# Optimization experiments

Hardware: AMD Instinct MI355X
Metric: run time of the kernel (lower is better)

Reference implementation:

```python
import jax, jax.numpy as jnp
from jax import lax
import numpy as np

V = 30000   # vocab_size
E = 64      # embedding_dim
H = 64      # lstm_units
K = 9       # num_tags
B = 512
T = 512


def setup_inputs() -> dict:
    key = jax.random.key(0)
    ks = jax.random.split(key, 12)
    s = 0.05
    return {
        "tokens": jax.random.randint(ks[0], (B, T), 0, V),
        "emb":   jax.random.normal(ks[1], (V + 1, E), dtype=jnp.float32) * s,
        "Wf": jax.random.normal(ks[2], (E, 4 * H), dtype=jnp.float32) * s,
        "Uf": jax.random.normal(ks[3], (H, 4 * H), dtype=jnp.float32) * s,
        "bf": jnp.zeros((4 * H,), dtype=jnp.float32),
        "Wb": jax.random.normal(ks[4], (E, 4 * H), dtype=jnp.float32) * s,
        "Ub": jax.random.normal(ks[5], (H, 4 * H), dtype=jnp.float32) * s,
        "bb": jnp.zeros((4 * H,), dtype=jnp.float32),
        "Wd": jax.random.normal(ks[6], (2 * H, K), dtype=jnp.float32) * s,
        "bd": jnp.zeros((K,), dtype=jnp.float32),
        "trans": jax.random.normal(ks[7], (K, K), dtype=jnp.float32) * s,
    }


def _lstm(x_tm, mask_tm, W, U, b):
    """Keras-convention LSTM over time-major x_tm [T,B,E]; masked steps carry state."""
    Bsz = x_tm.shape[1]
    h0 = jnp.zeros((Bsz, U.shape[0]), x_tm.dtype)
    c0 = jnp.zeros_like(h0)

    def step(carry, inp):
        h, c = carry
        xt, mt = inp                      # xt [B,E], mt [B] bool
        z = xt @ W + h @ U + b            # [B,4H], gate order i,f,g,o
        i, f, g, o = jnp.split(z, 4, axis=-1)
        c_new = jax.nn.sigmoid(f) * c + jax.nn.sigmoid(i) * jnp.tanh(g)
        h_new = jax.nn.sigmoid(o) * jnp.tanh(c_new)
        m = mt[:, None]
        h2 = jnp.where(m, h_new, h)
        c2 = jnp.where(m, c_new, c)
        return (h2, c2), h2

    _, hs = lax.scan(step, (h0, c0), (x_tm, mask_tm))
    return hs                              # [T,B,H]


def _viterbi(pot, mask, trans):
    """Batched Viterbi decode. pot [B,T,K], mask [B,T] bool, trans [K,K]."""
    pot_t = pot.transpose(1, 0, 2)         # [T,B,K]
    m_t = mask.T                           # [T,B]
    alpha0 = pot_t[0]
    ident = jnp.arange(K, dtype=jnp.int32)[None, :]

    def step(alpha, inp):
        p, m = inp                         # p [B,K], m [B]
        scores = alpha[:, :, None] + trans[None]   # [B, prev K, next K]
        best = scores.max(axis=1)
        bp = scores.argmax(axis=1).astype(jnp.int32)
        mm = m[:, None]
        alpha_new = jnp.where(mm, best + p, alpha)
        bp = jnp.where(mm, bp, ident)
        return alpha_new, bp

    alpha, bps = lax.scan(step, alpha0, (pot_t[1:], m_t[1:]))   # bps [T-1,B,K]
    last = alpha.argmax(axis=-1).astype(jnp.int32)              # [B]

    def back(tag, bp):
        prev = jnp.take_along_axis(bp, tag[:, None], axis=1)[:, 0]
        return prev, prev

    _, ys = lax.scan(back, last, bps, reverse=True)             # ys[t] = tag_t, t<T-1
    tags = jnp.concatenate([ys, last[None]], axis=0).T          # [B,T]
    return jnp.where(mask, tags, 0)


def reference(tokens, emb, Wf, Uf, bf, Wb, Ub, bb, Wd, bd, trans):
    mask = tokens != 0                     # mask_zero semantics
    x = emb[tokens]                        # [B,T,E]
    x_tm = x.transpose(1, 0, 2)            # [T,B,E]
    m_tm = mask.T
    hf = _lstm(x_tm, m_tm, Wf, Uf, bf)                     # forward dir
    hb = _lstm(x_tm[::-1], m_tm[::-1], Wb, Ub, bb)[::-1]   # backward dir
    h = jnp.concatenate([hf, hb], axis=-1).transpose(1, 0, 2)  # [B,T,2H]
    potentials = h @ Wd + bd               # CRF emission potentials [B,T,K]
    decoded = _viterbi(potentials, mask, trans)
    seq_len = mask.sum(axis=1).astype(jnp.int32)
    return decoded, potentials, seq_len
```

## Files before the change

kernel.cpp:

```cpp
#include <hip/hip_runtime.h>

#define BB 512
#define TT 512
#define KK 9
#define VP1 30001
#define BTK ((size_t)BB * TT * KK)

typedef __attribute__((ext_vector_type(8))) short short8;
typedef __attribute__((ext_vector_type(4))) float float4v;

__device__ __forceinline__ float sigm(float x) {
    return __builtin_amdgcn_rcpf(1.0f + __expf(-x));
}
__device__ __forceinline__ float tanh_(float x) {
    return 1.0f - 2.0f * __builtin_amdgcn_rcpf(__expf(2.0f * x) + 1.0f);
}

__device__ __forceinline__ unsigned short f2bf(float f) {
    unsigned int u = __float_as_uint(f);
    unsigned int r = u + 0x7fffu + ((u >> 16) & 1u);
    return (unsigned short)(r >> 16);
}
__device__ __forceinline__ float bflo2f(unsigned int d) { return __uint_as_float(d << 16); }
__device__ __forceinline__ float bfhi2f(unsigned int d) { return __uint_as_float(d & 0xffff0000u); }

__device__ __forceinline__ float bcast(float v, int i) {
    return __uint_as_float(__builtin_amdgcn_readlane(__float_as_uint(v), i));
}

__device__ __forceinline__ void block_sync_lds() {
    __builtin_amdgcn_s_waitcnt(0xC07F);
    __builtin_amdgcn_s_barrier();
}

__global__ __launch_bounds__(256, 1)
void embw_kernel(const float* __restrict__ emb,
                 const float* __restrict__ Wf, const float* __restrict__ bfv,
                 const float* __restrict__ Wb, const float* __restrict__ bbv,
                 unsigned short* __restrict__ embw)
{
    const int v0 = blockIdx.x * 64;
    const int tid = threadIdx.x;
    const int w = tid >> 6, lane = tid & 63;
    const int l16 = lane & 15, quad = lane >> 4;

    __shared__ __align__(16) unsigned short sm[512 * 72];
    __shared__ float blds[512];
    unsigned short (*wlds)[72]  = (unsigned short(*)[72])sm;
    unsigned short (*clds)[520] = (unsigned short(*)[520])sm;

#pragma unroll
    for (int it = 0; it < 128; ++it) {
        int idx = it * 256 + tid;
        int dir = idx >> 14, rem = idx & 16383;
        int k = rem >> 8, scol = rem & 255;
        int u = scol & 63, g = scol >> 6;
        float val = (dir ? Wb : Wf)[k * 256 + scol];
        wlds[dir * 256 + u * 4 + g][k] = f2bf(val);
    }
    {
        int c = tid, c2 = tid + 256;
        int dir0 = c >> 8, rem0 = c & 255;
        blds[c] = (dir0 ? bbv : bfv)[(rem0 & 3) * 64 + (rem0 >> 2)];
        int dir1 = c2 >> 8, rem1 = c2 & 255;
        blds[c2] = (dir1 ? bbv : bfv)[(rem1 & 3) * 64 + (rem1 >> 2)];
    }

    short8 aFr[4][2];
#pragma unroll
    for (int mt = 0; mt < 4; ++mt) {
        int vrow = v0 + mt * 16 + l16;
        if (vrow >= VP1) vrow = VP1 - 1;
        const float* er = emb + (size_t)vrow * 64;
#pragma unroll
        for (int q = 0; q < 2; ++q) {
            const float* p = er + q * 32 + quad * 8;
            float4 x0 = *(const float4*)(p);
            float4 x1 = *(const float4*)(p + 4);
            short8 v;
            v[0] = (short)f2bf(x0.x); v[1] = (short)f2bf(x0.y);
            v[2] = (short)f2bf(x0.z); v[3] = (short)f2bf(x0.w);
            v[4] = (short)f2bf(x1.x); v[5] = (short)f2bf(x1.y);
            v[6] = (short)f2bf(x1.z); v[7] = (short)f2bf(x1.w);
            aFr[mt][q] = v;
        }
    }
    __syncthreads();

    short8 bFr[8][2];
    float biasn[8];
#pragma unroll
    for (int n = 0; n < 8; ++n) {
        int c = w * 128 + n * 16 + l16;
        biasn[n] = blds[c];
#pragma unroll
        for (int q = 0; q < 2; ++q)
            bFr[n][q] = *(const short8*)&wlds[c][q * 32 + quad * 8];
    }

    float4v acc[4][8];
#pragma unroll
    for (int mt = 0; mt < 4; ++mt)
#pragma unroll
        for (int n = 0; n < 8; ++n) {
            acc[mt][n][0] = biasn[n]; acc[mt][n][1] = biasn[n];
            acc[mt][n][2] = biasn[n]; acc[mt][n][3] = biasn[n];
        }
#pragma unroll
    for (int mt = 0; mt < 4; ++mt)
#pragma unroll
        for (int n = 0; n < 8; ++n) {
            acc[mt][n] = __builtin_amdgcn_mfma_f32_16x16x32_bf16(aFr[mt][0], bFr[n][0], acc[mt][n], 0, 0, 0);
            acc[mt][n] = __builtin_amdgcn_mfma_f32_16x16x32_bf16(aFr[mt][1], bFr[n][1], acc[mt][n], 0, 0, 0);
        }

    __syncthreads();

#pragma unroll
    for (int mt = 0; mt < 4; ++mt)
#pragma unroll
        for (int n = 0; n < 8; ++n) {
            int cc = w * 128 + n * 16 + l16;
#pragma unroll
            for (int r = 0; r < 4; ++r)
                clds[mt * 16 + quad * 4 + r][cc] = f2bf(acc[mt][n][r]);
        }
    __syncthreads();

#pragma unroll
    for (int it = 0; it < 16; ++it) {
        int idx = it * 256 + tid;
        int row = idx >> 6, chunk = idx & 63;
        if (v0 + row < VP1) {
            uint4 val = *(const uint4*)&clds[row][chunk * 8];
            *(uint4*)(embw + (size_t)(v0 + row) * 512 + chunk * 8) = val;
        }
    }
}

__global__ __launch_bounds__(256, 1)
void rec_kernel(const int* __restrict__ tokens,
                const unsigned short* __restrict__ embw,
                const float* __restrict__ Uf, const float* __restrict__ Ub,
                const float* __restrict__ Wd,
                float* __restrict__ potf, float* __restrict__ potb)
{
    const int blk = blockIdx.x;
    const int dir = blk >> 7;
    const int row0 = (blk & 127) * 4;
    const int tid = threadIdx.x;
    const int lane = tid & 63;
    const int w = tid >> 6;
    const int l16 = lane & 15, quad = lane >> 4;
    const int u = w * 16 + l16;

    const float* Up = dir ? Ub : Uf;
    float* pot = dir ? potb : potf;
    const uint2* ebase = (const uint2*)embw + dir * 64 + u;

    __shared__ int tokl[4][TT];
    __shared__ __align__(16) unsigned short hl[2][16][72];

    for (int i = tid; i < 2 * 16 * 72; i += 256)
        ((unsigned short*)hl)[i] = 0;
    for (int i = tid; i < 4 * TT; i += 256) {
        int r = i >> 9, t = i & 511;
        tokl[r][t] = tokens[(row0 + r) * TT + t];
    }

    short8 bU[4][2];
#pragma unroll
    for (int g = 0; g < 4; ++g)
#pragma unroll
        for (int q = 0; q < 2; ++q) {
            short8 v;
#pragma unroll
            for (int j = 0; j < 8; ++j) {
                int k = q * 32 + quad * 8 + j;
                v[j] = (short)f2bf(Up[k * 256 + g * 64 + u]);
            }
            bU[g][q] = v;
        }
    short8 bW[2];
#pragma unroll
    for (int q = 0; q < 2; ++q) {
        short8 v;
#pragma unroll
        for (int j = 0; j < 8; ++j) {
            int k = q * 32 + quad * 8 + j;
            v[j] = (l16 < KK) ? (short)f2bf(Wd[(dir * 64 + k) * KK + l16]) : (short)0;
        }
        bW[q] = v;
    }

    __syncthreads();

    int tokA[4], tokB[4];
    uint2 zxp[4];
#pragma unroll
    for (int d = 0; d < 4; ++d) {
        int td = dir ? (TT - 1 - d) : d;
        int td4 = dir ? (TT - 1 - (d + 4)) : (d + 4);
        tokA[d] = tokl[quad][td];
        tokB[d] = tokl[quad][td4];
    }
#pragma unroll
    for (int d = 0; d < 4; ++d)
        zxp[d] = ebase[(size_t)tokA[d] << 7];

    float c_st = 0.f, h_st = 0.f;

    float4v accg[4];
#pragma unroll
    for (int g = 0; g < 4; ++g) {
        accg[g][0] = 0.f; accg[g][1] = 0.f; accg[g][2] = 0.f; accg[g][3] = 0.f;
    }

    const int tprev0 = dir ? (w == 0 ? TT - 4 : TT - w) : (w == 0 ? 3 : w - 1);
    int vOff = (((row0 + quad) * TT + tprev0) * KK + l16) * 4;
    const int vStep = (dir ? -4 : 4) * KK * 4;

    for (int sb = 0; sb < TT; sb += 4) {
#pragma unroll
        for (int ss = 0; ss < 4; ++ss) {
            const int s = sb + ss;
            int tcur = tokA[ss];
            uint2 zcur = zxp[ss];

            hl[ss & 1][quad * 4][u] = f2bf(h_st);

            if (s + 4 < TT)
                zxp[ss] = ebase[(size_t)tokB[ss] << 7];
            tokA[ss] = tokB[ss];

            block_sync_lds();

            const unsigned short* hrow = &hl[ss & 1][l16][0];
            short8 a0 = *(const short8*)(hrow + quad * 8);
            short8 a1 = *(const short8*)(hrow + 32 + quad * 8);

            if (s + 8 < TT) {
                int t8 = dir ? (TT - 1 - (s + 8)) : (s + 8);
                tokB[ss] = tokl[quad][t8];
            }

            accg[0][0] = bflo2f(zcur.x);
            accg[1][0] = bfhi2f(zcur.x);
            accg[2][0] = bflo2f(zcur.y);
            accg[3][0] = bfhi2f(zcur.y);
#pragma unroll
            for (int g = 0; g < 4; ++g) {
                accg[g] = __builtin_amdgcn_mfma_f32_16x16x32_bf16(a0, bU[g][0], accg[g], 0, 0, 0);
                accg[g] = __builtin_amdgcn_mfma_f32_16x16x32_bf16(a1, bU[g][1], accg[g], 0, 0, 0);
            }

            if (w == ss && s > 0) {
                float4v accP = {0.f, 0.f, 0.f, 0.f};
                accP = __builtin_amdgcn_mfma_f32_16x16x32_bf16(a0, bW[0], accP, 0, 0, 0);
                accP = __builtin_amdgcn_mfma_f32_16x16x32_bf16(a1, bW[1], accP, 0, 0, 0);
                if (l16 < KK)
                    *(float*)((char*)pot + vOff) = accP[0];
                vOff += vStep;
            }

            {
                float zi = accg[0][0], zf = accg[1][0], zg = accg[2][0], zo = accg[3][0];
                float cn = sigm(zf) * c_st + sigm(zi) * tanh_(zg);
                float hn = sigm(zo) * tanh_(cn);
                bool m = (tcur != 0);
                h_st = m ? hn : h_st;
                c_st = m ? cn : c_st;
            }
        }
    }

    hl[0][quad * 4][u] = f2bf(h_st);
    block_sync_lds();
    if (w == 0) {
        const unsigned short* hrow = &hl[0][l16][0];
        short8 a0 = *(const short8*)(hrow + quad * 8);
        short8 a1 = *(const short8*)(hrow + 32 + quad * 8);
        float4v accP = {0.f, 0.f, 0.f, 0.f};
        accP = __builtin_amdgcn_mfma_f32_16x16x32_bf16(a0, bW[0], accP, 0, 0, 0);
        accP = __builtin_amdgcn_mfma_f32_16x16x32_bf16(a1, bW[1], accP, 0, 0, 0);
        int tlast = dir ? 0 : (TT - 1);
        if (l16 < KK)
            pot[((size_t)(row0 + quad) * TT + tlast) * KK + l16] = accP[0];
    }
}

__global__ __launch_bounds__(64)
void viterbi_kernel(const int* __restrict__ tokens,
                    const float* __restrict__ potf, const float* __restrict__ potb,
                    const float* __restrict__ bd, const float* __restrict__ trans,
                    float* __restrict__ dec_out, float* __restrict__ pot_out,
                    float* __restrict__ seq_out)
{
    const int row = blockIdx.x;
    const int lane = threadIdx.x;

    __shared__ float pl[TT * KK];
    __shared__ unsigned char bpl[(TT - 1) * KK];
    __shared__ unsigned char maskl[TT];
    __shared__ unsigned char segmap[64][KK];
    __shared__ unsigned char bseq[65];
    __shared__ float decl_[TT];
    __shared__ float bdl[16];

    if (lane < KK) bdl[lane] = bd[lane];

    int cnt = 0;
#pragma unroll
    for (int ch = 0; ch < TT / 64; ++ch) {
        int tk = tokens[row * TT + ch * 64 + lane];
        int m = (tk != 0) ? 1 : 0;
        maskl[ch * 64 + lane] = (unsigned char)m;
        cnt += m;
    }
    for (int off = 32; off > 0; off >>= 1) cnt += __shfl_down(cnt, off);
    if (lane == 0) seq_out[row] = (float)cnt;

    const size_t base = (size_t)row * (TT * KK);
    int r9 = lane % KK;
    for (int i = 0; i < (TT * KK) / 64; ++i) {
        int li = i * 64 + lane;
        float s = potf[base + li] + potb[base + li] + bdl[r9];
        pl[li] = s;
        pot_out[base + li] = s;
        r9 = (r9 + 1 == KK) ? 0 : r9 + 1;
    }
    __syncthreads();

    float treg[KK];
#pragma unroll
    for (int i = 0; i < KK; ++i) treg[i] = (lane < KK) ? trans[i * KK + lane] : 0.f;

    float alpha = (lane < KK) ? pl[lane] : -1e30f;
    float pnext = (lane < KK) ? pl[KK + lane] : 0.f;
    int mnext = maskl[1];
    for (int t = 1; t < TT; ++t) {
        float p = pnext;
        int m = mnext;
        if (t + 1 < TT) {
            pnext = (lane < KK) ? pl[(t + 1) * KK + lane] : 0.f;
            mnext = maskl[t + 1];
        }
        float sc[KK];
#pragma unroll
        for (int i = 0; i < KK; ++i) sc[i] = bcast(alpha, i) + treg[i];
        float b0 = sc[0]; int i0 = 0;
        if (sc[1] > b0) { b0 = sc[1]; i0 = 1; }
        float b1 = sc[2]; int i1 = 2;
        if (sc[3] > b1) { b1 = sc[3]; i1 = 3; }
        float b2 = sc[4]; int i2 = 4;
        if (sc[5] > b2) { b2 = sc[5]; i2 = 5; }
        float b3 = sc[6]; int i3 = 6;
        if (sc[7] > b3) { b3 = sc[7]; i3 = 7; }
        if (b1 > b0) { b0 = b1; i0 = i1; }
        if (b3 > b2) { b2 = b3; i2 = i3; }
        if (b2 > b0) { b0 = b2; i0 = i2; }
        if (sc[8] > b0) { b0 = sc[8]; i0 = 8; }

        alpha = m ? (b0 + p) : alpha;
        int bpv = m ? i0 : lane;
        if (lane < KK) bpl[(t - 1) * KK + lane] = (unsigned char)bpv;
    }
    float sc[KK];
#pragma unroll
    for (int i = 0; i < KK; ++i) sc[i] = bcast(alpha, i);
    float b0 = sc[0]; int last = 0;
#pragma unroll
    for (int i = 1; i < KK; ++i)
        if (sc[i] > b0) { b0 = sc[i]; last = i; }
    __syncthreads();

    {
        int l = lane;
#pragma unroll
        for (int x = 0; x < KK; ++x) {
            int y = x;
#pragma unroll
            for (int d = 7; d >= 0; --d) {
                int t = 8 * l + d;
                if (t < TT - 1) y = bpl[t * KK + y];
            }
            segmap[l][x] = (unsigned char)y;
        }
    }
    __syncthreads();
    if (lane == 0) {
        int cur = last;
        bseq[64] = (unsigned char)last;
        for (int l = 63; l >= 0; --l) {
            cur = segmap[l][cur];
            bseq[l] = (unsigned char)cur;
        }
    }
    __syncthreads();
    {
        int l = lane;
        int cur = bseq[l + 1];
#pragma unroll
        for (int d = 7; d >= 0; --d) {
            int t = 8 * l + d;
            if (t < TT - 1) cur = bpl[t * KK + cur];
            decl_[t] = (maskl[t] != 0) ? (float)cur : 0.f;
        }
    }
    __syncthreads();
#pragma unroll
    for (int ch = 0; ch < TT / 64; ++ch)
        dec_out[(size_t)row * TT + ch * 64 + lane] = decl_[ch * 64 + lane];
}

extern "C" void kernel_launch(void* const* d_in, const int* in_sizes, int n_in,
                              void* d_out, int out_size, void* d_ws, size_t ws_size,
                              hipStream_t stream)
{
    const int*   tokens = (const int*)d_in[0];
    const float* emb    = (const float*)d_in[1];
    const float* Wf     = (const float*)d_in[2];
    const float* Uf     = (const float*)d_in[3];
    const float* bfv    = (const float*)d_in[4];
    const float* Wb     = (const float*)d_in[5];
    const float* Ub     = (const float*)d_in[6];
    const float* bbv    = (const float*)d_in[7];
    const float* Wd     = (const float*)d_in[8];
    const float* bd     = (const float*)d_in[9];
    const float* trans  = (const float*)d_in[10];

    float* out     = (float*)d_out;
    float* dec_out = out;
    float* pot_out = out + (size_t)BB * TT;
    float* seq_out = out + (size_t)BB * TT + BTK;

    float* potf = (float*)d_ws;
    float* potb = potf + BTK;
    unsigned short* embw = (unsigned short*)(potb + BTK);

    hipLaunchKernelGGL(embw_kernel, dim3(469), dim3(256), 0, stream,
                       emb, Wf, bfv, Wb, bbv, embw);
    hipLaunchKernelGGL(rec_kernel, dim3(256), dim3(256), 0, stream,
                       tokens, embw, Uf, Ub, Wd, potf, potb);
    hipLaunchKernelGGL(viterbi_kernel, dim3(BB), dim3(64), 0, stream,
                       tokens, potf, potb, bd, trans, dec_out, pot_out, seq_out);
}
```

Measured before the change: 399.4 us.

## Pre-swizzle input weights once, unroll Viterbi loop with branchless argmax

```diff
diff --git a/kernel.cpp b/kernel.cpp
--- a/kernel.cpp
+++ b/kernel.cpp
@@ -33,10 +33,34 @@
     __builtin_amdgcn_s_barrier();
 }
 
+__global__ __launch_bounds__(256)
+void wswz_kernel(const float* __restrict__ Wf, const float* __restrict__ bfv,
+                 const float* __restrict__ Wb, const float* __restrict__ bbv,
+                 unsigned short* __restrict__ wswz, float* __restrict__ bsw)
+{
+    const int tid = threadIdx.x;
+#pragma unroll
+    for (int it = 0; it < 16; ++it) {
+        int o = blockIdx.x * 4096 + it * 256 + tid;
+        int k = o & 63, c = o >> 6;
+        int dir = c >> 8, rem = c & 255;
+        int u = rem >> 2, g = rem & 3;
+        float val = (dir ? Wb : Wf)[k * 256 + g * 64 + u];
+        wswz[o] = f2bf(val);
+    }
+    if (blockIdx.x == 0) {
+#pragma unroll
+        for (int h = 0; h < 2; ++h) {
+            int c = h * 256 + tid;
+            int dir = c >> 8, rem = c & 255;
+            bsw[c] = (dir ? bbv : bfv)[(rem & 3) * 64 + (rem >> 2)];
+        }
+    }
+}
+
 __global__ __launch_bounds__(256, 1)
 void embw_kernel(const float* __restrict__ emb,
-                 const float* __restrict__ Wf, const float* __restrict__ bfv,
-                 const float* __restrict__ Wb, const float* __restrict__ bbv,
+                 const unsigned short* __restrict__ wswz, const float* __restrict__ bsw,
                  unsigned short* __restrict__ embw)
 {
     const int v0 = blockIdx.x * 64;
@@ -44,26 +68,18 @@
     const int w = tid >> 6, lane = tid & 63;
     const int l16 = lane & 15, quad = lane >> 4;
 
-    __shared__ __align__(16) unsigned short sm[512 * 72];
-    __shared__ float blds[512];
-    unsigned short (*wlds)[72]  = (unsigned short(*)[72])sm;
-    unsigned short (*clds)[520] = (unsigned short(*)[520])sm;
-
-#pragma unroll
-    for (int it = 0; it < 128; ++it) {
-        int idx = it * 256 + tid;
-        int dir = idx >> 14, rem = idx & 16383;
-        int k = rem >> 8, scol = rem & 255;
-        int u = scol & 63, g = scol >> 6;
-        float val = (dir ? Wb : Wf)[k * 256 + scol];
-        wlds[dir * 256 + u * 4 + g][k] = f2bf(val);
-    }
-    {
-        int c = tid, c2 = tid + 256;
-        int dir0 = c >> 8, rem0 = c & 255;
-        blds[c] = (dir0 ? bbv : bfv)[(rem0 & 3) * 64 + (rem0 >> 2)];
-        int dir1 = c2 >> 8, rem1 = c2 & 255;
-        blds[c2] = (dir1 ? bbv : bfv)[(rem1 & 3) * 64 + (rem1 >> 2)];
+    __shared__ __align__(16) unsigned short clds[64][520];
+
+    short8 bFr[8][2];
+    float biasn[8];
+#pragma unroll
+    for (int n = 0; n < 8; ++n) {
+        int c = w * 128 + n * 16 + l16;
+        biasn[n] = bsw[c];
+        const unsigned short* wp = wswz + c * 64;
+#pragma unroll
+        for (int q = 0; q < 2; ++q)
+            bFr[n][q] = *(const short8*)(wp + q * 32 + quad * 8);
     }
 
     short8 aFr[4][2];
@@ -85,18 +101,6 @@
             aFr[mt][q] = v;
         }
     }
-    __syncthreads();
-
-    short8 bFr[8][2];
-    float biasn[8];
-#pragma unroll
-    for (int n = 0; n < 8; ++n) {
-        int c = w * 128 + n * 16 + l16;
-        biasn[n] = blds[c];
-#pragma unroll
-        for (int q = 0; q < 2; ++q)
-            bFr[n][q] = *(const short8*)&wlds[c][q * 32 + quad * 8];
-    }
 
     float4v acc[4][8];
 #pragma unroll
@@ -113,8 +117,6 @@
             acc[mt][n] = __builtin_amdgcn_mfma_f32_16x16x32_bf16(aFr[mt][0], bFr[n][0], acc[mt][n], 0, 0, 0);
             acc[mt][n] = __builtin_amdgcn_mfma_f32_16x16x32_bf16(aFr[mt][1], bFr[n][1], acc[mt][n], 0, 0, 0);
         }
-
-    __syncthreads();
 
 #pragma unroll
     for (int mt = 0; mt < 4; ++mt)
@@ -299,15 +301,17 @@
     const int row = blockIdx.x;
     const int lane = threadIdx.x;
 
-    __shared__ float pl[TT * KK];
+    __shared__ float pl[TT * KK + 16];
     __shared__ unsigned char bpl[(TT - 1) * KK];
-    __shared__ unsigned char maskl[TT];
+    __shared__ unsigned char maskl[TT + 8];
     __shared__ unsigned char segmap[64][KK];
     __shared__ unsigned char bseq[65];
     __shared__ float decl_[TT];
     __shared__ float bdl[16];
 
     if (lane < KK) bdl[lane] = bd[lane];
+    if (lane < 8) maskl[TT + lane] = 0;
+    pl[TT * KK + lane % 16] = 0.f;
 
     int cnt = 0;
 #pragma unroll
@@ -338,28 +342,22 @@
     float alpha = (lane < KK) ? pl[lane] : -1e30f;
     float pnext = (lane < KK) ? pl[KK + lane] : 0.f;
     int mnext = maskl[1];
+#pragma unroll 4
     for (int t = 1; t < TT; ++t) {
         float p = pnext;
         int m = mnext;
-        if (t + 1 < TT) {
-            pnext = (lane < KK) ? pl[(t + 1) * KK + lane] : 0.f;
-            mnext = maskl[t + 1];
-        }
+        pnext = (lane < KK) ? pl[(t + 1) * KK + lane] : 0.f;
+        mnext = maskl[t + 1];
+
         float sc[KK];
 #pragma unroll
         for (int i = 0; i < KK; ++i) sc[i] = bcast(alpha, i) + treg[i];
-        float b0 = sc[0]; int i0 = 0;
-        if (sc[1] > b0) { b0 = sc[1]; i0 = 1; }
-        float b1 = sc[2]; int i1 = 2;
-        if (sc[3] > b1) { b1 = sc[3]; i1 = 3; }
-        float b2 = sc[4]; int i2 = 4;
-        if (sc[5] > b2) { b2 = sc[5]; i2 = 5; }
-        float b3 = sc[6]; int i3 = 6;
-        if (sc[7] > b3) { b3 = sc[7]; i3 = 7; }
-        if (b1 > b0) { b0 = b1; i0 = i1; }
-        if (b3 > b2) { b2 = b3; i2 = i3; }
-        if (b2 > b0) { b0 = b2; i0 = i2; }
-        if (sc[8] > b0) { b0 = sc[8]; i0 = 8; }
+        float b0 = fmaxf(fmaxf(fmaxf(sc[0], sc[1]), sc[2]),
+                   fmaxf(fmaxf(fmaxf(sc[3], sc[4]), sc[5]),
+                         fmaxf(fmaxf(sc[6], sc[7]), sc[8])));
+        int i0 = 8;
+#pragma unroll
+        for (int i = 7; i >= 0; --i) i0 = (sc[i] == b0) ? i : i0;
 
         alpha = m ? (b0 + p) : alpha;
         int bpv = m ? i0 : lane;
@@ -368,10 +366,12 @@
     float sc[KK];
 #pragma unroll
     for (int i = 0; i < KK; ++i) sc[i] = bcast(alpha, i);
-    float b0 = sc[0]; int last = 0;
-#pragma unroll
-    for (int i = 1; i < KK; ++i)
-        if (sc[i] > b0) { b0 = sc[i]; last = i; }
+    float b0 = fmaxf(fmaxf(fmaxf(sc[0], sc[1]), sc[2]),
+               fmaxf(fmaxf(fmaxf(sc[3], sc[4]), sc[5]),
+                     fmaxf(fmaxf(sc[6], sc[7]), sc[8])));
+    int last = 8;
+#pragma unroll
+    for (int i = 7; i >= 0; --i) last = (sc[i] == b0) ? i : last;
     __syncthreads();
 
     {
@@ -437,9 +437,13 @@
     float* potf = (float*)d_ws;
     float* potb = potf + BTK;
     unsigned short* embw = (unsigned short*)(potb + BTK);
-
+    unsigned short* wswz = (unsigned short*)potf;
+    float* bsw = (float*)((char*)potf + 512 * 64 * sizeof(unsigned short));
+
+    hipLaunchKernelGGL(wswz_kernel, dim3(8), dim3(256), 0, stream,
+                       Wf, bfv, Wb, bbv, wswz, bsw);
     hipLaunchKernelGGL(embw_kernel, dim3(469), dim3(256), 0, stream,
-                       emb, Wf, bfv, Wb, bbv, embw);
+                       emb, wswz, bsw, embw);
     hipLaunchKernelGGL(rec_kernel, dim3(256), dim3(256), 0, stream,
                        tokens, embw, Uf, Ub, Wd, potf, potb);
     hipLaunchKernelGGL(viterbi_kernel, dim3(BB), dim3(64), 0, stream,
```

Measured after the change: 398.1 us. Within noise of the previous version (-0.3%).
